# Kernel optimization log

Hardware: AMD Instinct MI355X
Metric: run time of the kernel (lower is better)

The kernel has to match this reference:

```python
import jax, jax.numpy as jnp
import numpy as np
import math

B, K, T = 4, 1024, 2048
OD, H = 128, 8


def setup_inputs() -> dict:
    key = jax.random.key(0)
    ks = jax.random.split(key, 6)
    s_in = 1.0 / math.sqrt(K)
    s_u = 1.0 / math.sqrt(H * OD)
    return {
        "x": jax.random.normal(ks[0], (B, K, T), dtype=jnp.float32),
        "Wk": jax.random.uniform(ks[1], (H * OD, K), minval=-s_in, maxval=s_in, dtype=jnp.float32),
        "Wq": jax.random.uniform(ks[2], (H * OD, K), minval=-s_in, maxval=s_in, dtype=jnp.float32),
        "Wv": jax.random.uniform(ks[3], (H * OD, K), minval=-s_in, maxval=s_in, dtype=jnp.float32),
        "Wu": jax.random.uniform(ks[4], (OD, H * OD), minval=-s_u, maxval=s_u, dtype=jnp.float32),
        "bu": jax.random.uniform(ks[5], (OD,), minval=-s_u, maxval=s_u, dtype=jnp.float32),
    }


def reference(x, Wk, Wq, Wv, Wu, bu):
    b, k, t = x.shape
    # QKV projections: Linear applied over channel dim of channels-first input
    keys = jnp.einsum('bkt,jk->bjt', x, Wk).reshape(b, H, OD, t)
    queries = jnp.einsum('bkt,jk->bjt', x, Wq).reshape(b, H, OD, t)
    values = jnp.einsum('bkt,jk->bjt', x, Wv).reshape(b, H, OD, t)
    # attention scores over time: [b, h, t, t]
    dot = jnp.einsum('bhkt,bhki->bhti', queries, keys) / math.sqrt(OD)
    dot = jax.nn.softmax(dot, axis=-1)
    out = jnp.einsum('bhti,bhki->bhkt', dot, values)  # [b, h, od, t]
    # unify heads: weight (OD, H*OD) viewed as (OD_out=k, H=h, OD=e)
    out = jnp.einsum('bhet,khe->bkt', out, Wu.reshape(OD, H, OD))
    return out + bu[None, :, None]
```

## Files before the change

### kernel.cpp

```cpp
#include <hip/hip_runtime.h>
#include <hip/hip_bf16.h>
#include <type_traits>
#include <utility>

#define DEVINL __device__ __forceinline__

typedef unsigned short u16;
typedef unsigned int   u32;
typedef short  s8v  __attribute__((ext_vector_type(8)));
typedef __bf16 b8v  __attribute__((ext_vector_type(8)));
typedef float  f4v  __attribute__((ext_vector_type(4)));
typedef float  f16v __attribute__((ext_vector_type(16)));

static constexpr int BB = 4, KD = 1024, TT = 2048, OD = 128, NH = 8;
static constexpr int J2 = 2048;

template<class V, class = void> struct mfma_takes : std::false_type {};
template<class V> struct mfma_takes<V, std::void_t<decltype(
    __builtin_amdgcn_mfma_f32_16x16x32_bf16(std::declval<V>(), std::declval<V>(),
                                            std::declval<f4v>(), 0, 0, 0))>> : std::true_type {};

template<class AV>
DEVINL f4v mfma16(AV a, AV b, f4v c) {
  if constexpr (mfma_takes<AV>::value) {
    return __builtin_amdgcn_mfma_f32_16x16x32_bf16(a, b, c, 0, 0, 0);
  } else {
    return __builtin_amdgcn_mfma_f32_16x16x32_bf16(
        __builtin_bit_cast(b8v, a), __builtin_bit_cast(b8v, b), c, 0, 0, 0);
  }
}

template<class V, class = void> struct mfma32_takes : std::false_type {};
template<class V> struct mfma32_takes<V, std::void_t<decltype(
    __builtin_amdgcn_mfma_f32_32x32x16_bf16(std::declval<V>(), std::declval<V>(),
                                            std::declval<f16v>(), 0, 0, 0))>> : std::true_type {};

template<class AV>
DEVINL f16v mfma32(AV a, AV b, f16v c) {
  if constexpr (mfma32_takes<AV>::value) {
    return __builtin_amdgcn_mfma_f32_32x32x16_bf16(a, b, c, 0, 0, 0);
  } else {
    return __builtin_amdgcn_mfma_f32_32x32x16_bf16(
        __builtin_bit_cast(b8v, a), __builtin_bit_cast(b8v, b), c, 0, 0, 0);
  }
}

DEVINL u16 f2bf(float f) {
  union { float f; u32 u; } v; v.f = f;
  u32 u = v.u;
  return (u16)((u + 0x7fffu + ((u >> 16) & 1u)) >> 16);
}
DEVINL float bf2f(u16 h) { union { u32 u; float f; } v; v.u = ((u32)h) << 16; return v.f; }

DEVINL u32 cvtpk_bf16(float a, float b) {
  u32 r;
  asm("v_cvt_pk_bf16_f32 %0, %1, %2" : "=v"(r) : "v"(a), "v"(b));
  return r;
}

DEVINL void gload_lds16(const void* g, void* l) {
  __builtin_amdgcn_global_load_lds(
      (const __attribute__((address_space(1))) void*)g,
      (__attribute__((address_space(3))) void*)l, 16, 0, 0);
}

__global__ void xpose_split_x(const float* __restrict__ x, u16* __restrict__ xTh) {
  __shared__ float tile[32][33];
  const int b  = blockIdx.z;
  const int k0 = blockIdx.y * 32;
  const int t0 = blockIdx.x * 32;
  const int tx = threadIdx.x;
  const int ty = threadIdx.y;
  const float* xb = x + (size_t)b * KD * TT;
#pragma unroll
  for (int j = 0; j < 4; ++j)
    tile[ty + j * 8][tx] = xb[(size_t)(k0 + ty + j * 8) * TT + t0 + tx];
  __syncthreads();
  u16* oh = xTh + (size_t)b * TT * KD;
#pragma unroll
  for (int j = 0; j < 4; ++j) {
    int t = ty + j * 8;
    float v = tile[tx][t];
    oh[(size_t)(t0 + t) * KD + k0 + tx] = f2bf(v);
  }
}

__global__ void split_weights(const float* __restrict__ Wk, const float* __restrict__ Wq,
                              const float* __restrict__ Wv, const float* __restrict__ Wu,
                              u16* __restrict__ Wkqh, u16* __restrict__ Wvh,
                              u16* __restrict__ Wuh,  u16* __restrict__ Wul,
                              float qscale) {
  int i = blockIdx.x * 256 + threadIdx.x;
  if (i < 1048576) {
    Wkqh[i] = f2bf(Wk[i]);
    Wkqh[1048576 + i] = f2bf(Wq[i] * qscale);
    Wvh[i] = f2bf(Wv[i]);
    if (i < 131072) {
      float v = Wu[i];  u16 hh = f2bf(v);
      Wuh[i] = hh;      Wul[i] = f2bf(v - bf2f(hh));
    }
  }
}

template<int EPI>
__global__ __launch_bounds__(256, 3) void gemm_bt_split(
    const u16* __restrict__ Ahi, const u16* __restrict__ Alo,
    const u16* __restrict__ Bhi, const u16* __restrict__ Blo,
    void* __restrict__ Couth,
    const float* __restrict__ bias,
    int Kdim, int ldc, long strideA, long strideB, long strideC, int npass) {
  __shared__ __align__(16) u16 At[128 * 64];
  __shared__ __align__(16) u16 Bt[128 * 64];
  const int tid = threadIdx.x;
  const int w = tid >> 6, l = tid & 63;
  const int wm = w >> 1, wn = w & 1;
  const int lr = l & 15, lg = l >> 4;
  const int b = blockIdx.z;
  const u16* Ah = Ahi + (size_t)b * strideA;
  const u16* Al = Alo ? Alo + (size_t)b * strideA : nullptr;
  const u16* Bh = Bhi + (size_t)b * strideB;
  const u16* Bl = Blo ? Blo + (size_t)b * strideB : nullptr;
  const int m0 = blockIdx.x * 128;
  const int n0 = (EPI == 3) ? ((blockIdx.y & 15) * 128) : (blockIdx.y * 128);
  const int ky = (EPI == 3) ? (blockIdx.y >> 4) : 0;
  const int kspan = (EPI == 3) ? (Kdim / 2) : Kdim;
  const int kbase = ky * kspan;

  int srow[4], soff[4];
#pragma unroll
  for (int i = 0; i < 4; ++i) {
    int c = tid + i * 256;
    int row = c >> 3, q = c & 7;
    srow[i] = row;
    soff[i] = (q ^ (row & 7)) * 8;
  }

  f4v acc[4][4] = {};

  const int spi = kspan / 64;
  const int iters = npass * spi;
  for (int it = 0; it < iters; ++it) {
    const int seg = it / spi;
    const int k = kbase + (it - seg * spi) * 64;
    const u16* As = (seg == 2) ? Al : Ah;
    const u16* Bs = (seg == 1) ? Bl : Bh;
#pragma unroll
    for (int i = 0; i < 4; ++i) {
      int c = tid + i * 256;
      gload_lds16(As + (size_t)(m0 + srow[i]) * Kdim + k + soff[i], (char*)At + c * 16);
      gload_lds16(Bs + (size_t)(n0 + srow[i]) * Kdim + k + soff[i], (char*)Bt + c * 16);
    }
    __syncthreads();
    __builtin_amdgcn_s_setprio(1);
#pragma unroll
    for (int kk = 0; kk < 2; ++kk) {
      const int q = kk * 4 + lg;
      s8v a[4], bb[4];
#pragma unroll
      for (int mi = 0; mi < 4; ++mi) {
        int row = wm * 64 + mi * 16 + lr;
        a[mi] = *(const s8v*)(&At[row * 64 + (q ^ (row & 7)) * 8]);
      }
#pragma unroll
      for (int ni = 0; ni < 4; ++ni) {
        int row = wn * 64 + ni * 16 + lr;
        bb[ni] = *(const s8v*)(&Bt[row * 64 + (q ^ (row & 7)) * 8]);
      }
#pragma unroll
      for (int mi = 0; mi < 4; ++mi)
#pragma unroll
        for (int ni = 0; ni < 4; ++ni)
          acc[mi][ni] = mfma16(a[mi], bb[ni], acc[mi][ni]);
    }
    __builtin_amdgcn_s_setprio(0);
    __syncthreads();
  }

  if constexpr (EPI == 2) {
    u16* Ch = (u16*)Couth + (size_t)b * strideC;
#pragma unroll
    for (int mi = 0; mi < 4; ++mi)
#pragma unroll
      for (int ni = 0; ni < 4; ++ni)
#pragma unroll
        for (int r = 0; r < 4; ++r) {
          int m = m0 + wm * 64 + mi * 16 + lg * 4 + r;
          int n = n0 + wn * 64 + ni * 16 + lr;
          Ch[(size_t)m * ldc + n] = f2bf(acc[mi][ni][r]);
        }
  } else if constexpr (EPI == 3) {
    float* C = (float*)Couth + ((size_t)ky * BB + b) * strideC;
#pragma unroll
    for (int mi = 0; mi < 4; ++mi)
#pragma unroll
      for (int ni = 0; ni < 4; ++ni)
#pragma unroll
        for (int r = 0; r < 4; ++r) {
          int m = m0 + wm * 64 + mi * 16 + lg * 4 + r;
          int n = n0 + wn * 64 + ni * 16 + lr;
          C[(size_t)m * ldc + n] = acc[mi][ni][r];
        }
  } else {
    float* C = (float*)Couth + (size_t)b * strideC;
#pragma unroll
    for (int mi = 0; mi < 4; ++mi)
#pragma unroll
      for (int ni = 0; ni < 4; ++ni)
#pragma unroll
        for (int r = 0; r < 4; ++r) {
          int m = m0 + wm * 64 + mi * 16 + lg * 4 + r;
          int n = n0 + wn * 64 + ni * 16 + lr;
          C[(size_t)m * ldc + n] = acc[mi][ni][r] + bias[m];
        }
  }
}

__global__ void addbias(const float* __restrict__ part, float* __restrict__ out,
                        const float* __restrict__ bias) {
  int i = blockIdx.x * 256 + threadIdx.x;
  f4v a = ((const f4v*)part)[i];
  f4v c = ((const f4v*)part)[i + 262144];
  float bs = bias[(i >> 9) & 127];
  f4v r;
#pragma unroll
  for (int j = 0; j < 4; ++j) r[j] = a[j] + c[j] + bs;
  ((f4v*)out)[i] = r;
}

__global__ __launch_bounds__(256, 2) void attn_fwd(
    const u16* __restrict__ QKTh, const u16* __restrict__ Vh,
    u16* __restrict__ OTh, u16* __restrict__ OTl) {
  __shared__ __align__(16) u16 Ksh[2][64 * 128];
  __shared__ __align__(16) u16 Vsh[2][128 * 64];
  __shared__ __align__(16) u16 Ph[128 * 64];

  const int bid = blockIdx.x;
  const int lid = (bid & 7) * 64 + (bid >> 3);
  const int t0 = (lid & 15) * 128;
  const int h  = (lid >> 4) & 7;
  const int b  = lid >> 7;

  const int tid = threadIdx.x;
  const int w = tid >> 6, l = tid & 63;
  const int lw = l & 31, hi = l >> 5;
  const size_t qb = (size_t)b * TT * J2;
  const u16* Qh_ = QKTh + qb + 1024 + h * 128;
  const u16* Kh_ = QKTh + qb + h * 128;
  const u16* Vh_ = Vh + (size_t)b * 1024 * TT + (size_t)h * 128 * TT;

  int koff[4], kdo[4], voff[4], vdo[4];
#pragma unroll
  for (int i = 0; i < 4; ++i) {
    int c = tid + i * 256;
    { int row = c >> 4, q = c & 15;
      koff[i] = row * J2 + (q ^ (row & 7)) * 8;  kdo[i] = c * 16; }
    { int row = c >> 3, q = c & 7;
      voff[i] = row * TT + (q ^ (row & 7)) * 8;  vdo[i] = c * 16; }
  }

#define ATTN_STAGE(BSEL, I0) do {                                          \
    _Pragma("unroll")                                                      \
    for (int i_ = 0; i_ < 4; ++i_) {                                       \
      gload_lds16(Kh_ + (size_t)(I0) * J2 + koff[i_], (char*)Ksh[BSEL] + kdo[i_]); \
      gload_lds16(Vh_ + voff[i_] + (I0),              (char*)Vsh[BSEL] + vdo[i_]); \
    } } while (0)

  s8v qh[8];
  {
    const size_t trow = (size_t)(t0 + w * 32 + lw) * J2;
#pragma unroll
    for (int st = 0; st < 8; ++st)
      qh[st] = *(const s8v*)(Qh_ + trow + st * 16 + hi * 8);
  }

  const int prow = (w * 32 + lw) * 128;
  const int pswz = (lw & 7) << 4;

  f16v o[4] = {};
  float mrow = -1e30f, lsum = 0.f;

  ATTN_STAGE(0, 0);

  for (int it = 0; it < 32; ++it) {
    const int cur = it & 1;
    if (it + 1 < 32) {
      ATTN_STAGE(cur ^ 1, (it + 1) * 64);
      asm volatile("s_waitcnt vmcnt(8)" ::: "memory");
    } else {
      asm volatile("s_waitcnt vmcnt(0)" ::: "memory");
    }
    __builtin_amdgcn_s_barrier();

    const u16* Ks = Ksh[cur];
    const u16* Vs = Vsh[cur];
    f16v s[2] = {};
    __builtin_amdgcn_s_setprio(1);
#pragma unroll
    for (int st = 0; st < 8; ++st) {
      const int sl = ((st * 2 + hi) ^ (lw & 7)) * 8;
      s8v k0 = *(const s8v*)(&Ks[lw * 128 + sl]);
      s8v k1 = *(const s8v*)(&Ks[(32 + lw) * 128 + sl]);
      s[0] = mfma32(k0, qh[st], s[0]);
      s[1] = mfma32(k1, qh[st], s[1]);
    }
    __builtin_amdgcn_s_setprio(0);

    float smax = s[0][0];
#pragma unroll
    for (int r = 1; r < 16; ++r) smax = fmaxf(smax, s[0][r]);
#pragma unroll
    for (int r = 0; r < 16; ++r) smax = fmaxf(smax, s[1][r]);
    smax = fmaxf(smax, __shfl_xor(smax, 32));

    if (__any(smax > mrow + 8.0f)) {
      float mn = fmaxf(mrow, smax);
      float al = exp2f(mrow - mn);
      mrow = mn;
      lsum *= al;
#pragma unroll
      for (int r = 0; r < 16; ++r) {
        float ar = __shfl(al, (r & 3) + 8 * (r >> 2) + 4 * hi);
#pragma unroll
        for (int et = 0; et < 4; ++et) o[et][r] *= ar;
      }
    }

    float p0[16], p1[16];
    float rsum = 0.f;
#pragma unroll
    for (int r = 0; r < 16; ++r) { p0[r] = exp2f(s[0][r] - mrow); rsum += p0[r]; }
#pragma unroll
    for (int r = 0; r < 16; ++r) { p1[r] = exp2f(s[1][r] - mrow); rsum += p1[r]; }
    rsum += __shfl_xor(rsum, 32);
    lsum += rsum;

#pragma unroll
    for (int g = 0; g < 4; ++g) {
      uint2 ta, tb;
      ta.x = cvtpk_bf16(p0[g * 4 + 0], p0[g * 4 + 1]);
      ta.y = cvtpk_bf16(p0[g * 4 + 2], p0[g * 4 + 3]);
      *(uint2*)((char*)Ph + prow + ((g * 16 + hi * 8) ^ pswz)) = ta;
      tb.x = cvtpk_bf16(p1[g * 4 + 0], p1[g * 4 + 1]);
      tb.y = cvtpk_bf16(p1[g * 4 + 2], p1[g * 4 + 3]);
      *(uint2*)((char*)Ph + prow + ((64 + g * 16 + hi * 8) ^ pswz)) = tb;
    }
    asm volatile("" ::: "memory");
    __builtin_amdgcn_sched_barrier(0);

    __builtin_amdgcn_s_setprio(1);
#pragma unroll
    for (int ks = 0; ks < 4; ++ks) {
      s8v pa = *(const s8v*)((char*)Ph + prow + (((ks * 2 + hi) * 16) ^ pswz));
#pragma unroll
      for (int et = 0; et < 4; ++et) {
        const int vrow = et * 32 + lw;
        s8v vh = *(const s8v*)(&Vs[vrow * 64 + (((ks * 2 + hi) ^ (lw & 7)) * 8)]);
        o[et] = mfma32(pa, vh, o[et]);
      }
    }
    __builtin_amdgcn_s_setprio(0);
    if (it + 1 < 32)
      __builtin_amdgcn_s_barrier();
  }
#undef ATTN_STAGE

  u16* oh = OTh + (size_t)b * TT * 1024;
  u16* ol = OTl + (size_t)b * TT * 1024;
#pragma unroll
  for (int r = 0; r < 16; ++r) {
    const int qrow = (r & 3) + 8 * (r >> 2) + 4 * hi;
    float ls = __shfl(lsum, qrow);
    float inv = 1.0f / ls;
    int t = t0 + w * 32 + qrow;
#pragma unroll
    for (int et = 0; et < 4; ++et) {
      int he = h * 128 + et * 32 + lw;
      float v = o[et][r] * inv;
      u16 hh = f2bf(v);
      oh[(size_t)t * 1024 + he] = hh;
      ol[(size_t)t * 1024 + he] = f2bf(v - bf2f(hh));
    }
  }
}

extern "C" void kernel_launch(void* const* d_in, const int* in_sizes, int n_in,
                              void* d_out, int out_size, void* d_ws, size_t ws_size,
                              hipStream_t stream) {
  const float* x  = (const float*)d_in[0];
  const float* Wk = (const float*)d_in[1];
  const float* Wq = (const float*)d_in[2];
  const float* Wv = (const float*)d_in[3];
  const float* Wu = (const float*)d_in[4];
  const float* bu = (const float*)d_in[5];
  float* out = (float*)d_out;

  const size_t need_bytes = 2ull * (8388608ull + 2097152ull + 1048576ull +
                                    131072ull * 2 + 16777216ull + 8388608ull +
                                    8388608ull * 2 + 4194304ull);
  if (ws_size < need_bytes) {
    hipMemsetAsync(d_out, 0, (size_t)out_size * sizeof(float), stream);
    return;
  }
  u16* p = (u16*)d_ws;
  u16* xTh = p;  p += 8388608;
  u16* Wkqh = p; p += 2097152;
  u16* Wvh = p;  p += 1048576;
  u16* Wuh = p;  p += 131072;
  u16* Wul = p;  p += 131072;
  u16* QKTh = p; p += 16777216;
  u16* Vh = p;   p += 8388608;
  u16* OTh = p;  p += 8388608;
  u16* OTl = p;  p += 8388608;
  float* Cpart = (float*)p; p += 4194304;

  const float qscale = 0.08838834764831845f * 1.4426950408889634f;

  xpose_split_x<<<dim3(64, 32, 4), dim3(32, 8), 0, stream>>>(x, xTh);
  split_weights<<<4096, 256, 0, stream>>>(Wk, Wq, Wv, Wu, Wkqh, Wvh, Wuh, Wul, qscale);

  gemm_bt_split<2><<<dim3(16, 16, 4), 256, 0, stream>>>(
      xTh, nullptr, Wkqh, nullptr, QKTh, nullptr,
      1024, 2048, 2097152L, 0L, 4194304L, 1);
  gemm_bt_split<2><<<dim3(8, 16, 4), 256, 0, stream>>>(
      Wvh, nullptr, xTh, nullptr, Vh, nullptr,
      1024, 2048, 0L, 2097152L, 2097152L, 1);
  attn_fwd<<<dim3(512), dim3(256), 0, stream>>>(QKTh, Vh, OTh, OTl);
  gemm_bt_split<3><<<dim3(1, 32, 4), 256, 0, stream>>>(
      Wuh, Wul, OTh, OTl, Cpart, nullptr,
      1024, 2048, 0L, 2097152L, 262144L, 3);
  addbias<<<1024, 256, 0, stream>>>(Cpart, out, bu);
}
```

Baseline: 200.4 us.

## Keep attention probabilities in registers via permlane32 swap, halve KV tile

Shrinks the attention KV tile from 64 to 32 keys per iteration and drops the shared-memory P buffer. Probabilities are repacked into MFMA A-operand layout directly in registers with v_permlane32_swap. With less LDS and fewer registers the launch bound rises to 3 blocks per CU. The intent is to remove the LDS round trip for P and raise occupancy, at the cost of twice as many loop iterations and barriers with a smaller prefetch per stage.

Result: no change. 201.0 us (+0.3%).

```diff
diff --git a/kernel.cpp b/kernel.cpp
--- a/kernel.cpp
+++ b/kernel.cpp
@@ -11,6 +11,7 @@
 typedef __bf16 b8v  __attribute__((ext_vector_type(8)));
 typedef float  f4v  __attribute__((ext_vector_type(4)));
 typedef float  f16v __attribute__((ext_vector_type(16)));
+typedef u32    u4v  __attribute__((ext_vector_type(4)));
 
 static constexpr int BB = 4, KD = 1024, TT = 2048, OD = 128, NH = 8;
 static constexpr int J2 = 2048;
@@ -227,12 +228,11 @@
   ((f4v*)out)[i] = r;
 }
 
-__global__ __launch_bounds__(256, 2) void attn_fwd(
+__global__ __launch_bounds__(256, 3) void attn_fwd(
     const u16* __restrict__ QKTh, const u16* __restrict__ Vh,
     u16* __restrict__ OTh, u16* __restrict__ OTl) {
-  __shared__ __align__(16) u16 Ksh[2][64 * 128];
-  __shared__ __align__(16) u16 Vsh[2][128 * 64];
-  __shared__ __align__(16) u16 Ph[128 * 64];
+  __shared__ __align__(16) u16 Ksh[2][32 * 128];
+  __shared__ __align__(16) u16 Vsh[2][128 * 32];
 
   const int bid = blockIdx.x;
   const int lid = (bid & 7) * 64 + (bid >> 3);
@@ -248,19 +248,19 @@
   const u16* Kh_ = QKTh + qb + h * 128;
   const u16* Vh_ = Vh + (size_t)b * 1024 * TT + (size_t)h * 128 * TT;
 
-  int koff[4], kdo[4], voff[4], vdo[4];
-#pragma unroll
-  for (int i = 0; i < 4; ++i) {
+  int koff[2], kdo[2], voff[2], vdo[2];
+#pragma unroll
+  for (int i = 0; i < 2; ++i) {
     int c = tid + i * 256;
     { int row = c >> 4, q = c & 15;
       koff[i] = row * J2 + (q ^ (row & 7)) * 8;  kdo[i] = c * 16; }
-    { int row = c >> 3, q = c & 7;
-      voff[i] = row * TT + (q ^ (row & 7)) * 8;  vdo[i] = c * 16; }
+    { int row = c >> 2, q = c & 3;
+      voff[i] = row * TT + (q ^ ((row >> 1) & 3)) * 8;  vdo[i] = c * 16; }
   }
 
 #define ATTN_STAGE(BSEL, I0) do {                                          \
     _Pragma("unroll")                                                      \
-    for (int i_ = 0; i_ < 4; ++i_) {                                       \
+    for (int i_ = 0; i_ < 2; ++i_) {                                       \
       gload_lds16(Kh_ + (size_t)(I0) * J2 + koff[i_], (char*)Ksh[BSEL] + kdo[i_]); \
       gload_lds16(Vh_ + voff[i_] + (I0),              (char*)Vsh[BSEL] + vdo[i_]); \
     } } while (0)
@@ -273,19 +273,16 @@
       qh[st] = *(const s8v*)(Qh_ + trow + st * 16 + hi * 8);
   }
 
-  const int prow = (w * 32 + lw) * 128;
-  const int pswz = (lw & 7) << 4;
-
   f16v o[4] = {};
   float mrow = -1e30f, lsum = 0.f;
 
   ATTN_STAGE(0, 0);
 
-  for (int it = 0; it < 32; ++it) {
+  for (int it = 0; it < 64; ++it) {
     const int cur = it & 1;
-    if (it + 1 < 32) {
-      ATTN_STAGE(cur ^ 1, (it + 1) * 64);
-      asm volatile("s_waitcnt vmcnt(8)" ::: "memory");
+    if (it + 1 < 64) {
+      ATTN_STAGE(cur ^ 1, (it + 1) * 32);
+      asm volatile("s_waitcnt vmcnt(4)" ::: "memory");
     } else {
       asm volatile("s_waitcnt vmcnt(0)" ::: "memory");
     }
@@ -293,23 +290,18 @@
 
     const u16* Ks = Ksh[cur];
     const u16* Vs = Vsh[cur];
-    f16v s[2] = {};
+    f16v s = {};
     __builtin_amdgcn_s_setprio(1);
 #pragma unroll
     for (int st = 0; st < 8; ++st) {
-      const int sl = ((st * 2 + hi) ^ (lw & 7)) * 8;
-      s8v k0 = *(const s8v*)(&Ks[lw * 128 + sl]);
-      s8v k1 = *(const s8v*)(&Ks[(32 + lw) * 128 + sl]);
-      s[0] = mfma32(k0, qh[st], s[0]);
-      s[1] = mfma32(k1, qh[st], s[1]);
+      s8v kf = *(const s8v*)(&Ks[lw * 128 + (((st * 2 + hi) ^ (lw & 7)) * 8)]);
+      s = mfma32(kf, qh[st], s);
     }
     __builtin_amdgcn_s_setprio(0);
 
-    float smax = s[0][0];
-#pragma unroll
-    for (int r = 1; r < 16; ++r) smax = fmaxf(smax, s[0][r]);
-#pragma unroll
-    for (int r = 0; r < 16; ++r) smax = fmaxf(smax, s[1][r]);
+    float smax = s[0];
+#pragma unroll
+    for (int r = 1; r < 16; ++r) smax = fmaxf(smax, s[r]);
     smax = fmaxf(smax, __shfl_xor(smax, 32));
 
     if (__any(smax > mrow + 8.0f)) {
@@ -325,41 +317,42 @@
       }
     }
 
-    float p0[16], p1[16];
     float rsum = 0.f;
 #pragma unroll
-    for (int r = 0; r < 16; ++r) { p0[r] = exp2f(s[0][r] - mrow); rsum += p0[r]; }
-#pragma unroll
-    for (int r = 0; r < 16; ++r) { p1[r] = exp2f(s[1][r] - mrow); rsum += p1[r]; }
+    for (int r = 0; r < 16; ++r) { s[r] = exp2f(s[r] - mrow); rsum += s[r]; }
     rsum += __shfl_xor(rsum, 32);
     lsum += rsum;
 
+    u32 wp[4][2];
 #pragma unroll
     for (int g = 0; g < 4; ++g) {
-      uint2 ta, tb;
-      ta.x = cvtpk_bf16(p0[g * 4 + 0], p0[g * 4 + 1]);
-      ta.y = cvtpk_bf16(p0[g * 4 + 2], p0[g * 4 + 3]);
-      *(uint2*)((char*)Ph + prow + ((g * 16 + hi * 8) ^ pswz)) = ta;
-      tb.x = cvtpk_bf16(p1[g * 4 + 0], p1[g * 4 + 1]);
-      tb.y = cvtpk_bf16(p1[g * 4 + 2], p1[g * 4 + 3]);
-      *(uint2*)((char*)Ph + prow + ((64 + g * 16 + hi * 8) ^ pswz)) = tb;
-    }
-    asm volatile("" ::: "memory");
-    __builtin_amdgcn_sched_barrier(0);
+      wp[g][0] = cvtpk_bf16(s[g * 4 + 0], s[g * 4 + 1]);
+      wp[g][1] = cvtpk_bf16(s[g * 4 + 2], s[g * 4 + 3]);
+    }
+    s8v pa[2];
+#pragma unroll
+    for (int ks = 0; ks < 2; ++ks) {
+      u32 a0 = wp[2 * ks][0], b0 = wp[2 * ks + 1][0];
+      u32 a1 = wp[2 * ks][1], b1 = wp[2 * ks + 1][1];
+      asm volatile("v_permlane32_swap_b32 %0, %1" : "+v"(a0), "+v"(b0));
+      asm volatile("v_permlane32_swap_b32 %0, %1" : "+v"(a1), "+v"(b1));
+      u4v fw; fw[0] = a0; fw[1] = a1; fw[2] = b0; fw[3] = b1;
+      pa[ks] = __builtin_bit_cast(s8v, fw);
+    }
 
     __builtin_amdgcn_s_setprio(1);
 #pragma unroll
-    for (int ks = 0; ks < 4; ++ks) {
-      s8v pa = *(const s8v*)((char*)Ph + prow + (((ks * 2 + hi) * 16) ^ pswz));
+    for (int ks = 0; ks < 2; ++ks) {
 #pragma unroll
       for (int et = 0; et < 4; ++et) {
         const int vrow = et * 32 + lw;
-        s8v vh = *(const s8v*)(&Vs[vrow * 64 + (((ks * 2 + hi) ^ (lw & 7)) * 8)]);
-        o[et] = mfma32(pa, vh, o[et]);
+        s8v vh = *(const s8v*)(&Vs[vrow * 32 +
+                                   (((ks * 2 + hi) ^ ((vrow >> 1) & 3)) * 8)]);
+        o[et] = mfma32(pa[ks], vh, o[et]);
       }
     }
     __builtin_amdgcn_s_setprio(0);
-    if (it + 1 < 32)
+    if (it + 1 < 64)
       __builtin_amdgcn_s_barrier();
   }
 #undef ATTN_STAGE
```
